# Kernel optimization log

Measured on AMD Instinct MI355X. Metric: run time of the kernel, lower is better.

Reference implementation:

```python
import jax, jax.numpy as jnp
import numpy as np

B, S, D = 2, 2048, 1024
H, KH, HD = 16, 4, 64          # n_heads, n_kv_heads, head_dim
REP = H // KH                  # GQA repeat factor
ROPE_THETA = 10000.0


def _rope(x, cos, sin):
    """x: [B,S,nh,HD]; cos/sin: [S,HD//2]. Interleaved-pair complex rotation."""
    xr = x.reshape(*x.shape[:-1], HD // 2, 2)
    x0, x1 = xr[..., 0], xr[..., 1]
    c = cos[None, :, None, :]  # [1,S,1,HD//2]
    s = sin[None, :, None, :]
    o0 = x0 * c - x1 * s
    o1 = x0 * s + x1 * c
    return jnp.stack([o0, o1], axis=-1).reshape(x.shape)


def setup_inputs() -> dict:
    key = jax.random.key(0)
    ks = jax.random.split(key, 5)
    x = jax.random.normal(ks[0], (B, S, D), dtype=jnp.float32)
    sc = 0.02
    wq = jax.random.normal(ks[1], (D, H * HD), dtype=jnp.float32) * sc
    wk = jax.random.normal(ks[2], (D, KH * HD), dtype=jnp.float32) * sc
    wv = jax.random.normal(ks[3], (D, KH * HD), dtype=jnp.float32) * sc
    wo = jax.random.normal(ks[4], (H * HD, D), dtype=jnp.float32) * sc
    # RoPE tables (precomputed buffers in the torch model)
    inv_freq = 1.0 / (ROPE_THETA ** (np.arange(0, HD, 2, dtype=np.float32) / HD))
    ang = np.arange(S, dtype=np.float32)[:, None] * inv_freq[None, :]  # [S,HD//2]
    freqs_cos = jnp.asarray(np.cos(ang))
    freqs_sin = jnp.asarray(np.sin(ang))
    # additive causal mask [1,1,S,S]
    neg = jnp.finfo(jnp.float32).min
    mask = jnp.where(jnp.tril(jnp.ones((S, S), dtype=bool)), 0.0, neg)[None, None]
    return {"x": x, "wq": wq, "wk": wk, "wv": wv, "wo": wo,
            "freqs_cos": freqs_cos, "freqs_sin": freqs_sin, "mask": mask}


def reference(x, wq, wk, wv, wo, freqs_cos, freqs_sin, mask):
    scale = 1.0 / jnp.sqrt(jnp.float32(HD))
    q = (x @ wq).reshape(B, S, H, HD)
    k = (x @ wk).reshape(B, S, KH, HD)
    v = (x @ wv).reshape(B, S, KH, HD)
    q = _rope(q, freqs_cos, freqs_sin)
    k = _rope(k, freqs_cos, freqs_sin)
    # GQA: query head h uses kv head h // REP == grouping consecutive q heads
    q = q.reshape(B, S, KH, REP, HD).transpose(0, 2, 3, 1, 4)  # [B,KH,REP,S,HD]
    k = k.transpose(0, 2, 1, 3)                                # [B,KH,S,HD]
    v = v.transpose(0, 2, 1, 3)
    scores = jnp.einsum('bkrqd,bksd->bkrqs', q, k) * scale     # [B,KH,REP,S,S]
    scores = scores + mask[:, :, None]                         # broadcast over REP
    attn = jax.nn.softmax(scores, axis=-1)
    out = jnp.einsum('bkrqs,bksd->bkrqd', attn, v)             # [B,KH,REP,S,HD]
    out = out.transpose(0, 3, 1, 2, 4).reshape(B, S, H * HD)
    return out @ wo
```

## Files before the change

### kernel.cpp

```cpp
#include <hip/hip_runtime.h>
#include <hip/hip_bf16.h>

using bf16 = __hip_bfloat16;
typedef short bf16x8 __attribute__((ext_vector_type(8)));
typedef float f32x4 __attribute__((ext_vector_type(4)));

#define CB 2
#define CS 2048
#define CD 1024
#define CH 16
#define CKH 4
#define CHD 64
#define CREP 4
#define CNQ (CH*CHD)
#define CNKV (CKH*CHD)
#define CM (CB*CS)

__device__ __forceinline__ unsigned short f2bf(float f) {
  union { float f; unsigned int i; } c; c.f = f;
  unsigned int r = c.i + 0x7FFFu + ((c.i >> 16) & 1u);
  return (unsigned short)(r >> 16);
}
__device__ __forceinline__ float bf2f(unsigned short u) {
  union { unsigned int i; float f; } c;
  c.i = ((unsigned int)u) << 16;
  return c.f;
}
__device__ __forceinline__ void gload_lds16(const void* g, void* l) {
  __builtin_amdgcn_global_load_lds(
      (const __attribute__((address_space(1))) void*)g,
      (__attribute__((address_space(3))) void*)l, 16, 0, 0);
}

__global__ __launch_bounds__(256) void gemm_mfma_kernel(
    const bf16* __restrict__ A, const bf16* __restrict__ Bt,
    float* __restrict__ C, int Mm, int Nn, int Kk, int lda)
{
  __shared__ __align__(16) bf16 As[2][64 * 64];
  __shared__ __align__(16) bf16 Bs[2][128 * 64];
  const int tid = threadIdx.x;
  const int lane = tid & 63;
  const int l15 = lane & 15;
  const int g = lane >> 4;
  const int wid = tid >> 6;
  const int wr = (wid >> 1) * 32;
  const int wc = (wid & 1) * 64;
  const int m0 = blockIdx.x * 64;
  const int n0 = blockIdx.y * 128;

  f32x4 acc[2][4];
  #pragma unroll
  for (int i = 0; i < 2; ++i)
    #pragma unroll
    for (int j = 0; j < 4; ++j)
      acc[i][j] = (f32x4){0.f, 0.f, 0.f, 0.f};

  const int slr = tid >> 3;
  const int scg = (tid & 7) ^ (slr & 7);
  const bf16* aStage = A + (size_t)(m0 + slr) * lda + scg * 8;
  const bf16* bStage = Bt + (size_t)(n0 + slr) * Kk + scg * 8;
  char* aDst = (char*)As + wid * 1024;
  char* bDst = (char*)Bs + wid * 1024;

#define GSTAGE(bi, k0) do {                                                   \
    gload_lds16(aStage + (k0),                      aDst + (bi) * 8192);      \
    gload_lds16(aStage + 32 * (size_t)lda + (k0),   aDst + (bi) * 8192 + 4096); \
    gload_lds16(bStage + (k0),                      bDst + (bi) * 16384);     \
    gload_lds16(bStage + 32 * (size_t)Kk + (k0),    bDst + (bi) * 16384 + 4096); \
    gload_lds16(bStage + 64 * (size_t)Kk + (k0),    bDst + (bi) * 16384 + 8192); \
    gload_lds16(bStage + 96 * (size_t)Kk + (k0),    bDst + (bi) * 16384 + 12288); \
  } while (0)

  const int nt = Kk >> 6;
  int bi = 0;
  GSTAGE(0, 0);
  for (int t = 0; t < nt; ++t) {
    if (t + 1 < nt) {
      GSTAGE(bi ^ 1, (t + 1) * 64);
      asm volatile("s_waitcnt vmcnt(6)" ::: "memory");
    } else {
      asm volatile("s_waitcnt vmcnt(0)" ::: "memory");
    }
    __builtin_amdgcn_s_barrier();
    asm volatile("" ::: "memory");

    const char* AB = (const char*)As + bi * 8192;
    const char* BB = (const char*)Bs + bi * 16384;
    bf16x8 af[2][2], bfr[4][2];
    #pragma unroll
    for (int mt = 0; mt < 2; ++mt) {
      int row = wr + mt * 16 + l15;
      #pragma unroll
      for (int c = 0; c < 2; ++c)
        af[mt][c] = *(const bf16x8*)(AB + row * 128 + (((c * 4 + g) ^ (row & 7)) << 4));
    }
    #pragma unroll
    for (int nt2 = 0; nt2 < 4; ++nt2) {
      int row = wc + nt2 * 16 + l15;
      #pragma unroll
      for (int c = 0; c < 2; ++c)
        bfr[nt2][c] = *(const bf16x8*)(BB + row * 128 + (((c * 4 + g) ^ (row & 7)) << 4));
    }
    #pragma unroll
    for (int c = 0; c < 2; ++c)
      #pragma unroll
      for (int mt = 0; mt < 2; ++mt)
        #pragma unroll
        for (int nt2 = 0; nt2 < 4; ++nt2)
          acc[mt][nt2] = __builtin_amdgcn_mfma_f32_16x16x32_bf16(af[mt][c], bfr[nt2][c], acc[mt][nt2], 0, 0, 0);

    asm volatile("" ::: "memory");
    __builtin_amdgcn_s_barrier();
    bi ^= 1;
  }
#undef GSTAGE

  #pragma unroll
  for (int mt = 0; mt < 2; ++mt)
    #pragma unroll
    for (int r4 = 0; r4 < 4; ++r4) {
      const size_t row = (size_t)(m0 + wr + mt * 16 + 4 * g + r4);
      #pragma unroll
      for (int nt2 = 0; nt2 < 4; ++nt2)
        C[row * Nn + n0 + wc + nt2 * 16 + l15] = acc[mt][nt2][r4];
    }
}

__global__ __launch_bounds__(256) void gemm_qkv_rope_kernel(
    const bf16* __restrict__ A, const bf16* __restrict__ Bt,
    const float* __restrict__ fc, const float* __restrict__ fs,
    bf16* __restrict__ qb, bf16* __restrict__ kb, bf16* __restrict__ vt)
{
  __shared__ __align__(16) bf16 As[2][64 * 64];
  __shared__ __align__(16) bf16 Bs[2][128 * 64];
  const int tid = threadIdx.x;
  const int lane = tid & 63;
  const int l15 = lane & 15;
  const int g = lane >> 4;
  const int wid = tid >> 6;
  const int wr = (wid >> 1) * 32;
  const int wc = (wid & 1) * 64;
  const int m0 = blockIdx.x * 64;
  const int n0 = blockIdx.y * 128;
  const int Kk = CD;

  f32x4 acc[2][4];
  #pragma unroll
  for (int i = 0; i < 2; ++i)
    #pragma unroll
    for (int j = 0; j < 4; ++j)
      acc[i][j] = (f32x4){0.f, 0.f, 0.f, 0.f};

  const int slr = tid >> 3;
  const int scg = (tid & 7) ^ (slr & 7);
  const bf16* aStage = A + (size_t)(m0 + slr) * Kk + scg * 8;
  const bf16* bStage = Bt + (size_t)(n0 + slr) * Kk + scg * 8;
  char* aDst = (char*)As + wid * 1024;
  char* bDst = (char*)Bs + wid * 1024;

#define GSTAGE(bi, k0) do {                                                   \
    gload_lds16(aStage + (k0),                      aDst + (bi) * 8192);      \
    gload_lds16(aStage + 32 * (size_t)Kk + (k0),    aDst + (bi) * 8192 + 4096); \
    gload_lds16(bStage + (k0),                      bDst + (bi) * 16384);     \
    gload_lds16(bStage + 32 * (size_t)Kk + (k0),    bDst + (bi) * 16384 + 4096); \
    gload_lds16(bStage + 64 * (size_t)Kk + (k0),    bDst + (bi) * 16384 + 8192); \
    gload_lds16(bStage + 96 * (size_t)Kk + (k0),    bDst + (bi) * 16384 + 12288); \
  } while (0)

  const int nt = Kk >> 6;
  int bi = 0;
  GSTAGE(0, 0);
  for (int t = 0; t < nt; ++t) {
    if (t + 1 < nt) {
      GSTAGE(bi ^ 1, (t + 1) * 64);
      asm volatile("s_waitcnt vmcnt(6)" ::: "memory");
    } else {
      asm volatile("s_waitcnt vmcnt(0)" ::: "memory");
    }
    __builtin_amdgcn_s_barrier();
    asm volatile("" ::: "memory");

    const char* AB = (const char*)As + bi * 8192;
    const char* BB = (const char*)Bs + bi * 16384;
    bf16x8 af[2][2], bfr[4][2];
    #pragma unroll
    for (int mt = 0; mt < 2; ++mt) {
      int row = wr + mt * 16 + l15;
      #pragma unroll
      for (int c = 0; c < 2; ++c)
        af[mt][c] = *(const bf16x8*)(AB + row * 128 + (((c * 4 + g) ^ (row & 7)) << 4));
    }
    #pragma unroll
    for (int nt2 = 0; nt2 < 4; ++nt2) {
      int row = wc + nt2 * 16 + l15;
      #pragma unroll
      for (int c = 0; c < 2; ++c)
        bfr[nt2][c] = *(const bf16x8*)(BB + row * 128 + (((c * 4 + g) ^ (row & 7)) << 4));
    }
    #pragma unroll
    for (int c = 0; c < 2; ++c)
      #pragma unroll
      for (int mt = 0; mt < 2; ++mt)
        #pragma unroll
        for (int nt2 = 0; nt2 < 4; ++nt2)
          acc[mt][nt2] = __builtin_amdgcn_mfma_f32_16x16x32_bf16(af[mt][c], bfr[nt2][c], acc[mt][nt2], 0, 0, 0);

    asm volatile("" ::: "memory");
    __builtin_amdgcn_s_barrier();
    bi ^= 1;
  }
#undef GSTAGE

  if (blockIdx.y < 10) {
    const bool isq = (blockIdx.y < 8);
    const float qsc = isq ? 0.18033688f : 1.0f;
    #pragma unroll
    for (int mt = 0; mt < 2; ++mt)
      #pragma unroll
      for (int r4 = 0; r4 < 4; ++r4) {
        int m = m0 + wr + mt * 16 + 4 * g + r4;
        int s = m & (CS - 1), bb = m >> 11;
        #pragma unroll
        for (int nt2 = 0; nt2 < 4; ++nt2) {
          int n = n0 + wc + nt2 * 16 + l15;
          int d = n & 63;
          float val = acc[mt][nt2][r4];
          float par = __shfl_xor(val, 1, 64);
          float cv = fc[s * 32 + (d >> 1)];
          float sv = fs[s * 32 + (d >> 1)];
          float o = (d & 1) ? (par * sv + val * cv) : (val * cv - par * sv);
          o *= qsc;
          if (isq) {
            int h = n >> 6;
            ((unsigned short*)qb)[(((size_t)bb * CH + h) * CS + s) * CHD + d] = f2bf(o);
          } else {
            int kh = (n >> 6) - 16;
            ((unsigned short*)kb)[(((size_t)bb * CKH + kh) * CS + s) * CHD + d] = f2bf(o);
          }
        }
      }
  } else {
    #pragma unroll
    for (int mt = 0; mt < 2; ++mt) {
      int mb = m0 + wr + mt * 16 + 4 * g;
      int s0 = mb & (CS - 1), bb = mb >> 11;
      #pragma unroll
      for (int nt2 = 0; nt2 < 4; ++nt2) {
        int n = n0 + wc + nt2 * 16 + l15;
        int d = n & 63;
        int kh = (n >> 6) - 20;
        ushort4 pk = make_ushort4(f2bf(acc[mt][nt2][0]), f2bf(acc[mt][nt2][1]),
                                  f2bf(acc[mt][nt2][2]), f2bf(acc[mt][nt2][3]));
        *(ushort4*)&((unsigned short*)vt)[(((size_t)bb * CKH + kh) * CHD + d) * CS + s0] = pk;
      }
    }
  }
}

__global__ __launch_bounds__(256) void prep_kernel(
    const float* __restrict__ x, bf16* __restrict__ xb,
    const float* __restrict__ wq, const float* __restrict__ wk,
    const float* __restrict__ wv, const float* __restrict__ wo,
    bf16* __restrict__ wqkvt, bf16* __restrict__ wot)
{
  const int tid = threadIdx.x;
  int bid = blockIdx.x;
  if (bid < 2048) {
    int i = (bid * 256 + tid) * 8;
    float4 a = *(const float4*)&x[i];
    float4 b = *(const float4*)&x[i + 4];
    unsigned short* o = (unsigned short*)xb + i;
    *(ushort4*)o = make_ushort4(f2bf(a.x), f2bf(a.y), f2bf(a.z), f2bf(a.w));
    *(ushort4*)(o + 4) = make_ushort4(f2bf(b.x), f2bf(b.y), f2bf(b.z), f2bf(b.w));
    return;
  }
  bid -= 2048;
  const float* W; bf16* Wt; int Nn, bx, by;
  if (bid < 256)      { W = wq; Wt = wqkvt;                      Nn = 1024; bx = bid & 15;        by = bid >> 4; }
  else if (bid < 320) { W = wk; Wt = wqkvt + (size_t)1024 * CD;  Nn = 256;  bx = (bid-256) & 15;  by = (bid-256) >> 4; }
  else if (bid < 384) { W = wv; Wt = wqkvt + (size_t)1280 * CD;  Nn = 256;  bx = (bid-320) & 15;  by = (bid-320) >> 4; }
  else                { W = wo; Wt = wot;                        Nn = 1024; bx = (bid-384) & 15;  by = (bid-384) >> 4; }
  const int Kk = 1024;
  const int k0 = bx * 64;
  const int n0 = by * 64;

  __shared__ float T[64][65];
  const int lr = tid >> 4;
  const int lc = (tid & 15) * 4;
  #pragma unroll
  for (int i = 0; i < 4; ++i) {
    float4 v = *(const float4*)&W[(size_t)(k0 + lr + i * 16) * Nn + n0 + lc];
    T[lr + i * 16][lc + 0] = v.x;
    T[lr + i * 16][lc + 1] = v.y;
    T[lr + i * 16][lc + 2] = v.z;
    T[lr + i * 16][lc + 3] = v.w;
  }
  __syncthreads();
  const int rn = tid >> 3;
  const int ck = (tid & 7) * 8;
  #pragma unroll
  for (int i = 0; i < 2; ++i) {
    int nn = rn + i * 32;
    unsigned short u[8];
    #pragma unroll
    for (int e = 0; e < 8; ++e) u[e] = f2bf(T[ck + e][nn]);
    unsigned short* dst = (unsigned short*)Wt + (size_t)(n0 + nn) * Kk + k0 + ck;
    *(ushort4*)dst = make_ushort4(u[0], u[1], u[2], u[3]);
    *(ushort4*)(dst + 4) = make_ushort4(u[4], u[5], u[6], u[7]);
  }
}

__global__ __launch_bounds__(256, 2) void flash_split_kernel(
    const bf16* __restrict__ qb, const bf16* __restrict__ kb,
    const bf16* __restrict__ vt, bf16* __restrict__ oc0,
    bf16* __restrict__ ob, float2* __restrict__ ml)
{
  __shared__ __align__(16) char arena[51200];
  char* KL = arena;
  char* VL = arena + 16384;
  const int tid = threadIdx.x;
  const int lane = tid & 63;
  const int wid = tid >> 6;
  unsigned short* PLW = (unsigned short*)(arena + 32768) + wid * 2304;
  const int l15 = lane & 15;
  const int g = lane >> 4;
  const int blk = blockIdx.x;
  const int chunk = blk & 1;
  const int grp = (blk >> 1) & 7;
  const int idx = blk >> 4;
  const int qt = 63 - idx;
  const int kh = grp & 3;
  const int b = grp >> 2;
  const int h = kh * CREP + wid;
  const int N64 = (qt >> 1) + 1;
  const int hc = N64 >> 1;
  const int tbeg = chunk ? hc : 0;
  const int tend = chunk ? N64 : hc;

  const bf16* qbase = qb + ((size_t)(b * CH + h) * CS + qt * 32) * CHD;
  const bf16* kbase = kb + (size_t)(b * CKH + kh) * CS * CHD;
  const bf16* vbase = vt + (size_t)(b * CKH + kh) * CHD * CS;

  bf16x8 qf[2][2];
  #pragma unroll
  for (int qs = 0; qs < 2; ++qs)
    #pragma unroll
    for (int c = 0; c < 2; ++c)
      qf[qs][c] = *(const bf16x8*)(qbase + (qs * 16 + l15) * CHD + c * 32 + g * 8);

  bf16x8 ones;
  #pragma unroll
  for (int e = 0; e < 8; ++e) ones[e] = (short)0x3F80;

  f32x4 oacc[2][4];
  f32x4 lacc[2];
  #pragma unroll
  for (int qs = 0; qs < 2; ++qs) {
    lacc[qs] = (f32x4){0.f, 0.f, 0.f, 0.f};
    #pragma unroll
    for (int dt = 0; dt < 4; ++dt)
      oacc[qs][dt] = (f32x4){0.f, 0.f, 0.f, 0.f};
  }
  float mrow[2] = {-1e30f, -1e30f};

  const int slr = tid >> 3;
  const int scg = (tid & 7) ^ (slr & 7);
  const bf16* kstage = kbase + (size_t)slr * CHD + scg * 8;
  const bf16* vstage = vbase + (size_t)slr * CS + scg * 8;
  char* kdst = KL + wid * 1024;
  char* vdst = VL + wid * 1024;

#define STAGE(bi, t64) do {                                        \
    const bf16* ks_ = kstage + (size_t)(t64) * 64 * CHD;           \
    const bf16* vs_ = vstage + (t64) * 64;                         \
    gload_lds16(ks_,            kdst + (bi) * 8192);               \
    gload_lds16(ks_ + 32 * CHD, kdst + (bi) * 8192 + 4096);        \
    gload_lds16(vs_,            vdst + (bi) * 8192);               \
    gload_lds16(vs_ + 32 * CS,  vdst + (bi) * 8192 + 4096);        \
  } while (0)

  if (tbeg < tend) {
    int bi = 0;
    STAGE(0, tbeg);
    for (int t = tbeg; t < tend; ++t) {
      if (t + 1 < tend) {
        STAGE(bi ^ 1, t + 1);
        asm volatile("s_waitcnt vmcnt(4)" ::: "memory");
      } else {
        asm volatile("s_waitcnt vmcnt(0)" ::: "memory");
      }
      __builtin_amdgcn_s_barrier();
      asm volatile("" ::: "memory");

      const char* KB = KL + bi * 8192;
      const char* VB = VL + bi * 8192;
      bf16x8 kfr[4][2], vfr[4][2];
      #pragma unroll
      for (int kt = 0; kt < 4; ++kt) {
        int row = kt * 16 + l15;
        #pragma unroll
        for (int c = 0; c < 2; ++c)
          kfr[kt][c] = *(const bf16x8*)(KB + row * 128 + (((c * 4 + g) ^ (row & 7)) << 4));
      }
      #pragma unroll
      for (int dt = 0; dt < 4; ++dt) {
        int row = dt * 16 + l15;
        #pragma unroll
        for (int st = 0; st < 2; ++st)
          vfr[dt][st] = *(const bf16x8*)(VB + row * 128 + (((st * 4 + g) ^ (row & 7)) << 4));
      }

      f32x4 sacc[4][2];
      #pragma unroll
      for (int kt = 0; kt < 4; ++kt)
        #pragma unroll
        for (int qs = 0; qs < 2; ++qs)
          sacc[kt][qs] = (f32x4){0.f, 0.f, 0.f, 0.f};
      __builtin_amdgcn_s_setprio(1);
      #pragma unroll
      for (int c = 0; c < 2; ++c)
        #pragma unroll
        for (int kt = 0; kt < 4; ++kt)
          #pragma unroll
          for (int qs = 0; qs < 2; ++qs)
            sacc[kt][qs] = __builtin_amdgcn_mfma_f32_16x16x32_bf16(kfr[kt][c], qf[qs][c], sacc[kt][qs], 0, 0, 0);
      __builtin_amdgcn_s_setprio(0);

      const bool diag = (t == N64 - 1);
      #pragma unroll
      for (int qs = 0; qs < 2; ++qs) {
        float pe[16];
        float pm = -1e30f;
        #pragma unroll
        for (int kt = 0; kt < 4; ++kt)
          #pragma unroll
          for (int r = 0; r < 4; ++r) {
            float v = sacc[kt][qs][r];
            if (diag) {
              int koff = t * 64 + kt * 16 + 4 * g + r;
              if (koff > qt * 32 + qs * 16 + l15) v = -1e30f;
            }
            pe[kt * 4 + r] = v;
            pm = fmaxf(pm, v);
          }
        if (__any(pm > mrow[qs] + 8.0f)) {
          pm = fmaxf(pm, __shfl_xor(pm, 16, 64));
          pm = fmaxf(pm, __shfl_xor(pm, 32, 64));
          float nm = fmaxf(mrow[qs], pm);
          float corr = exp2f(mrow[qs] - nm);
          mrow[qs] = nm;
          lacc[qs] *= corr;
          #pragma unroll
          for (int dt = 0; dt < 4; ++dt) oacc[qs][dt] *= corr;
        }
        #pragma unroll
        for (int i = 0; i < 16; ++i)
          pe[i] = exp2f(pe[i] - mrow[qs]);
        #pragma unroll
        for (int kt = 0; kt < 4; ++kt) {
          unsigned int lo = (__float_as_uint(pe[kt * 4 + 1]) & 0xFFFF0000u) |
                            (__float_as_uint(pe[kt * 4 + 0]) >> 16);
          unsigned int hi = (__float_as_uint(pe[kt * 4 + 3]) & 0xFFFF0000u) |
                            (__float_as_uint(pe[kt * 4 + 2]) >> 16);
          *(uint2*)&PLW[(qs * 16 + l15) * 72 + kt * 16 + 4 * g] = make_uint2(lo, hi);
        }
      }

      __builtin_amdgcn_s_setprio(1);
      #pragma unroll
      for (int qs = 0; qs < 2; ++qs) {
        #pragma unroll
        for (int st = 0; st < 2; ++st) {
          bf16x8 pf = *(const bf16x8*)&PLW[(qs * 16 + l15) * 72 + st * 32 + g * 8];
          lacc[qs] = __builtin_amdgcn_mfma_f32_16x16x32_bf16(ones, pf, lacc[qs], 0, 0, 0);
          #pragma unroll
          for (int dt = 0; dt < 4; ++dt)
            oacc[qs][dt] = __builtin_amdgcn_mfma_f32_16x16x32_bf16(vfr[dt][st], pf, oacc[qs][dt], 0, 0, 0);
        }
      }
      __builtin_amdgcn_s_setprio(0);

      asm volatile("" ::: "memory");
      __builtin_amdgcn_s_barrier();
      bi ^= 1;
    }
  }
#undef STAGE

  unsigned short* pdst = (unsigned short*)(chunk ? ob : oc0);
  #pragma unroll
  for (int qs = 0; qs < 2; ++qs) {
    int qg = qt * 32 + qs * 16 + l15;
    unsigned short* prow = pdst + (size_t)(b * CS + qg) * CNQ + h * CHD;
    #pragma unroll
    for (int dt = 0; dt < 4; ++dt)
      *(ushort4*)&prow[dt * 16 + 4 * g] =
          make_ushort4(f2bf(oacc[qs][dt][0]), f2bf(oacc[qs][dt][1]),
                       f2bf(oacc[qs][dt][2]), f2bf(oacc[qs][dt][3]));
    if (g == 0)
      ml[(((size_t)chunk * CB + b) * CH + h) * CS + qg] = make_float2(mrow[qs], lacc[qs][0]);
  }
}

__global__ __launch_bounds__(256) void merge_kernel(
    const bf16* __restrict__ oc0, bf16* __restrict__ ob,
    const float2* __restrict__ ml)
{
  const int e8 = blockIdx.x * 256 + threadIdx.x;
  const size_t off = (size_t)e8 * 8;
  const int row = (int)(off >> 10);
  const int col = (int)(off & 1023);
  const int h = col >> 6;
  const int b = row >> 11;
  const int s = row & (CS - 1);
  float2 ml0 = ml[(((size_t)0 * CB + b) * CH + h) * CS + s];
  float2 ml1 = ml[(((size_t)1 * CB + b) * CH + h) * CS + s];
  float M = fmaxf(ml0.x, ml1.x);
  float c0 = exp2f(ml0.x - M), c1 = exp2f(ml1.x - M);
  float inv = 1.0f / (c0 * ml0.y + c1 * ml1.y);
  ushort4 a0 = *(const ushort4*)((const unsigned short*)oc0 + off);
  ushort4 a1 = *(const ushort4*)((const unsigned short*)oc0 + off + 4);
  ushort4 b0 = *(const ushort4*)((const unsigned short*)ob + off);
  ushort4 b1 = *(const ushort4*)((const unsigned short*)ob + off + 4);
  unsigned short r[8];
  const unsigned short* p0 = &a0.x;
  const unsigned short* p1 = &b0.x;
  #pragma unroll
  for (int i = 0; i < 4; ++i)
    r[i] = f2bf((c0 * bf2f(p0[i]) + c1 * bf2f(p1[i])) * inv);
  p0 = &a1.x; p1 = &b1.x;
  #pragma unroll
  for (int i = 0; i < 4; ++i)
    r[4 + i] = f2bf((c0 * bf2f(p0[i]) + c1 * bf2f(p1[i])) * inv);
  *(ushort4*)((unsigned short*)ob + off) = make_ushort4(r[0], r[1], r[2], r[3]);
  *(ushort4*)((unsigned short*)ob + off + 4) = make_ushort4(r[4], r[5], r[6], r[7]);
}

extern "C" void kernel_launch(void* const* d_in, const int* in_sizes, int n_in,
                              void* d_out, int out_size, void* d_ws, size_t ws_size,
                              hipStream_t stream)
{
  const float* x  = (const float*)d_in[0];
  const float* wq = (const float*)d_in[1];
  const float* wk = (const float*)d_in[2];
  const float* wv = (const float*)d_in[3];
  const float* wo = (const float*)d_in[4];
  const float* fc = (const float*)d_in[5];
  const float* fs = (const float*)d_in[6];
  float* out = (float*)d_out;

  char* ws = (char*)d_ws;
  bf16*   x_b   = (bf16*)(ws);
  bf16*   wqkvt = (bf16*)(ws + 8388608);
  bf16*   wot   = (bf16*)(ws + 11534336);
  bf16*   q_b   = (bf16*)(ws + 13631488);
  bf16*   k_b   = (bf16*)(ws + 22020096);
  bf16*   v_t   = (bf16*)(ws + 24117248);
  bf16*   o_b   = (bf16*)(ws);
  bf16*   oc0   = (bf16*)(ws + 26214400);
  float2* mlb   = (float2*)(ws + 34603008);

  prep_kernel<<<2688, 256, 0, stream>>>(x, x_b, wq, wk, wv, wo, wqkvt, wot);
  gemm_qkv_rope_kernel<<<dim3(64, 12), 256, 0, stream>>>(x_b, wqkvt, fc, fs, q_b, k_b, v_t);
  flash_split_kernel<<<1024, 256, 0, stream>>>(q_b, k_b, v_t, oc0, o_b, mlb);
  merge_kernel<<<2048, 256, 0, stream>>>(oc0, o_b, mlb);
  gemm_mfma_kernel<<<dim3(64, 8), 256, 0, stream>>>(o_b, wot, out, CM, CD, CNQ, CNQ);
}
```

Measured before the change: 106.0 us.

## Feed P directly from registers into 16x16x16 MFMA, dropping LDS round-trip

In the flash-attention kernel the softmax probabilities no longer go through a per-wave LDS buffer. Each S-accumulator tile is packed in registers into a bf16x4 fragment and fed straight into 16x16x16 bf16 MFMAs for both the PV product and the row-sum. To match, V fragments are reloaded as 4-element pieces with adjusted swizzle offsets. This removes the LDS store/load of P and cuts shared memory from 51200 to 32768 bytes, which may allow higher occupancy, but it doubles the MFMA instruction count by using the smaller K=16 instruction; the setprio hints are also dropped.

```diff
diff --git a/kernel.cpp b/kernel.cpp
--- a/kernel.cpp
+++ b/kernel.cpp
@@ -3,6 +3,7 @@
 
 using bf16 = __hip_bfloat16;
 typedef short bf16x8 __attribute__((ext_vector_type(8)));
+typedef short bf16x4 __attribute__((ext_vector_type(4)));
 typedef float f32x4 __attribute__((ext_vector_type(4)));
 
 #define CB 2
@@ -30,6 +31,16 @@
   __builtin_amdgcn_global_load_lds(
       (const __attribute__((address_space(1))) void*)g,
       (__attribute__((address_space(3))) void*)l, 16, 0, 0);
+}
+__device__ __forceinline__ f32x4 mfma16bf16(bf16x4 a, bf16x4 b, f32x4 c) {
+#if __has_builtin(__builtin_amdgcn_mfma_f32_16x16x16_bf16)
+  return __builtin_amdgcn_mfma_f32_16x16x16_bf16(a, b, c, 0, 0, 0);
+#elif __has_builtin(__builtin_amdgcn_mfma_f32_16x16x16bf16_1k)
+  return __builtin_amdgcn_mfma_f32_16x16x16bf16_1k(a, b, c, 0, 0, 0);
+#else
+  asm("v_mfma_f32_16x16x16_bf16 %0, %1, %2, %0" : "+v"(c) : "v"(a), "v"(b));
+  return c;
+#endif
 }
 
 __global__ __launch_bounds__(256) void gemm_mfma_kernel(
@@ -315,13 +326,12 @@
     const bf16* __restrict__ vt, bf16* __restrict__ oc0,
     bf16* __restrict__ ob, float2* __restrict__ ml)
 {
-  __shared__ __align__(16) char arena[51200];
+  __shared__ __align__(16) char arena[32768];
   char* KL = arena;
   char* VL = arena + 16384;
   const int tid = threadIdx.x;
   const int lane = tid & 63;
   const int wid = tid >> 6;
-  unsigned short* PLW = (unsigned short*)(arena + 32768) + wid * 2304;
   const int l15 = lane & 15;
   const int g = lane >> 4;
   const int blk = blockIdx.x;
@@ -348,9 +358,9 @@
     for (int c = 0; c < 2; ++c)
       qf[qs][c] = *(const bf16x8*)(qbase + (qs * 16 + l15) * CHD + c * 32 + g * 8);
 
-  bf16x8 ones;
-  #pragma unroll
-  for (int e = 0; e < 8; ++e) ones[e] = (short)0x3F80;
+  bf16x4 ones4;
+  #pragma unroll
+  for (int e = 0; e < 4; ++e) ones4[e] = (short)0x3F80;
 
   f32x4 oacc[2][4];
   f32x4 lacc[2];
@@ -394,7 +404,7 @@
 
       const char* KB = KL + bi * 8192;
       const char* VB = VL + bi * 8192;
-      bf16x8 kfr[4][2], vfr[4][2];
+      bf16x8 kfr[4][2];
       #pragma unroll
       for (int kt = 0; kt < 4; ++kt) {
         int row = kt * 16 + l15;
@@ -402,12 +412,14 @@
         for (int c = 0; c < 2; ++c)
           kfr[kt][c] = *(const bf16x8*)(KB + row * 128 + (((c * 4 + g) ^ (row & 7)) << 4));
       }
+      bf16x4 vfr16[4][4];
       #pragma unroll
       for (int dt = 0; dt < 4; ++dt) {
         int row = dt * 16 + l15;
         #pragma unroll
-        for (int st = 0; st < 2; ++st)
-          vfr[dt][st] = *(const bf16x8*)(VB + row * 128 + (((st * 4 + g) ^ (row & 7)) << 4));
+        for (int kt = 0; kt < 4; ++kt)
+          vfr16[dt][kt] = *(const bf16x4*)(VB + row * 128 +
+              (((2 * kt + (g >> 1)) ^ (row & 7)) << 4) + (g & 1) * 8);
       }
 
       f32x4 sacc[4][2];
@@ -416,7 +428,6 @@
         #pragma unroll
         for (int qs = 0; qs < 2; ++qs)
           sacc[kt][qs] = (f32x4){0.f, 0.f, 0.f, 0.f};
-      __builtin_amdgcn_s_setprio(1);
       #pragma unroll
       for (int c = 0; c < 2; ++c)
         #pragma unroll
@@ -424,7 +435,6 @@
           #pragma unroll
           for (int qs = 0; qs < 2; ++qs)
             sacc[kt][qs] = __builtin_amdgcn_mfma_f32_16x16x32_bf16(kfr[kt][c], qf[qs][c], sacc[kt][qs], 0, 0, 0);
-      __builtin_amdgcn_s_setprio(0);
 
       const bool diag = (t == N64 - 1);
       #pragma unroll
@@ -458,27 +468,17 @@
           pe[i] = exp2f(pe[i] - mrow[qs]);
         #pragma unroll
         for (int kt = 0; kt < 4; ++kt) {
-          unsigned int lo = (__float_as_uint(pe[kt * 4 + 1]) & 0xFFFF0000u) |
-                            (__float_as_uint(pe[kt * 4 + 0]) >> 16);
-          unsigned int hi = (__float_as_uint(pe[kt * 4 + 3]) & 0xFFFF0000u) |
-                            (__float_as_uint(pe[kt * 4 + 2]) >> 16);
-          *(uint2*)&PLW[(qs * 16 + l15) * 72 + kt * 16 + 4 * g] = make_uint2(lo, hi);
+          union { uint2 u; bf16x4 v; } cv;
+          cv.u.x = (__float_as_uint(pe[kt * 4 + 1]) & 0xFFFF0000u) |
+                   (__float_as_uint(pe[kt * 4 + 0]) >> 16);
+          cv.u.y = (__float_as_uint(pe[kt * 4 + 3]) & 0xFFFF0000u) |
+                   (__float_as_uint(pe[kt * 4 + 2]) >> 16);
+          lacc[qs] = mfma16bf16(ones4, cv.v, lacc[qs]);
+          #pragma unroll
+          for (int dt = 0; dt < 4; ++dt)
+            oacc[qs][dt] = mfma16bf16(vfr16[dt][kt], cv.v, oacc[qs][dt]);
         }
       }
-
-      __builtin_amdgcn_s_setprio(1);
-      #pragma unroll
-      for (int qs = 0; qs < 2; ++qs) {
-        #pragma unroll
-        for (int st = 0; st < 2; ++st) {
-          bf16x8 pf = *(const bf16x8*)&PLW[(qs * 16 + l15) * 72 + st * 32 + g * 8];
-          lacc[qs] = __builtin_amdgcn_mfma_f32_16x16x32_bf16(ones, pf, lacc[qs], 0, 0, 0);
-          #pragma unroll
-          for (int dt = 0; dt < 4; ++dt)
-            oacc[qs][dt] = __builtin_amdgcn_mfma_f32_16x16x32_bf16(vfr[dt][st], pf, oacc[qs][dt], 0, 0, 0);
-        }
-      }
-      __builtin_amdgcn_s_setprio(0);
 
       asm volatile("" ::: "memory");
       __builtin_amdgcn_s_barrier();
```

Result: faster. 98.90 us (-6.7%).
